# Performance work log

Measured on AMD Instinct MI355X. Metric: run time of the kernel, lower is better.

Reference implementation:

```python
import math
import jax, jax.numpy as jnp
import numpy as np

B_IN, B_OUT = 16, 16
F_IN, F_OUT, BATCH = 32, 64, 4
N_ALPHA, N_GAMMA = 4, 3
KERNEL_BETA = math.pi / 8.0
L_TOT = sum((2 * l + 1) ** 2 for l in range(B_OUT))  # 5456


def _lg(n):
    return math.lgamma(n + 1.0)


def _small_d(l, beta):
    """Wigner small-d matrix d^l_{m,n}(beta), [2l+1, 2l+1], Condon-Shortley phase."""
    c, s = math.cos(0.5 * beta), math.sin(0.5 * beta)
    d = np.zeros((2 * l + 1, 2 * l + 1), dtype=np.float64)
    for mi, m in enumerate(range(-l, l + 1)):
        for ni, n in enumerate(range(-l, l + 1)):
            pref = 0.5 * (_lg(l + m) + _lg(l - m) + _lg(l + n) + _lg(l - n))
            acc = 0.0
            for k in range(max(0, n - m), min(l + n, l - m) + 1):
                ln = pref - _lg(l + n - k) - _lg(k) - _lg(m - n + k) - _lg(l - m - k)
                acc += ((-1.0) ** (m - n + k)) * math.exp(ln) * (c ** (2 * l + n - m - 2 * k)) * (s ** (m - n + 2 * k))
            d[mi, ni] = acc
    return d


def _qweights(b):
    """Kostelec-Rockmore SOFT quadrature weights over the 2b beta samples."""
    k = np.arange(b)
    w = np.array([
        (2.0 / b) * math.sin(math.pi * (2 * j + 1) / (4.0 * b)) *
        np.sum(np.sin((2 * j + 1) * (2 * k + 1) * math.pi / (4.0 * b)) / (2 * k + 1))
        for j in range(2 * b)])
    return w


def _wigner_table(betas, b_out, scale_fn):
    rows = []
    for beta in betas:
        blocks = [(_small_d(l, beta) * scale_fn(l)).ravel() for l in range(b_out)]
        rows.append(np.concatenate(blocks))
    return np.stack(rows)  # [len(betas), L_TOT]


def _grid_basis(grid, b_out):
    """conj(D^l_{mn}(a,b,g)) = e^{+i m a} d^l_{mn}(b) e^{+i n g}, flattened over (l,m,n)."""
    cols = []
    for (a, bb, g) in grid:
        blocks = []
        for l in range(b_out):
            m = np.arange(-l, l + 1)
            d = _small_d(l, bb)
            ph = np.exp(1j * (m[:, None] * a + m[None, :] * g))
            blocks.append((d * ph).ravel())
        cols.append(np.concatenate(blocks))
    return np.stack(cols, axis=1)  # [L_TOT, n_grid] complex


def _freq_indices(b_out, nfft):
    ms, ns = [], []
    for l in range(b_out):
        r = np.arange(-l, l + 1)
        M, N = np.meshgrid(r, r, indexing='ij')
        ms.append(np.mod(M.ravel(), nfft))
        ns.append(np.mod(N.ravel(), nfft))
    return np.concatenate(ms), np.concatenate(ns)


def make_grid():
    alphas = [2.0 * math.pi * i / N_ALPHA for i in range(N_ALPHA)]
    gammas = [2.0 * math.pi * i / N_GAMMA for i in range(N_GAMMA)]
    return [(a, KERNEL_BETA, g) for a in alphas for g in gammas]


def setup_inputs() -> dict:
    key = jax.random.key(0)
    k1, k2 = jax.random.split(key)
    x = jax.random.normal(k1, (BATCH, F_IN, 2 * B_IN, 2 * B_IN, 2 * B_IN), jnp.float32)
    grid = make_grid()
    n_grid = len(grid)
    stdv = 1.0 / math.sqrt(n_grid * F_IN * (B_OUT ** 3) / float(B_IN ** 3))
    kernel = stdv * jax.random.normal(k2, (F_IN, F_OUT, n_grid), jnp.float32)
    bias = jnp.zeros((1, F_OUT, 1, 1, 1), jnp.float32)
    # analysis table: quadrature weight * d, with (2pi/2b)^2/(8pi^2) = 1/(8 b^2) absorbed
    betas_in = np.pi * (2 * np.arange(2 * B_IN) + 1) / (4.0 * B_IN)
    w = _qweights(B_IN) / (8.0 * B_IN ** 2)
    wig_f = _wigner_table(betas_in, B_OUT, lambda l: 1.0) * w[:, None]
    # synthesis table: (2l+1) * d, times (2b)^2 to cancel ifft2 normalization
    betas_out = np.pi * (2 * np.arange(2 * B_OUT) + 1) / (4.0 * B_OUT)
    wig_i = _wigner_table(betas_out, B_OUT, lambda l: (2 * l + 1) * (2 * B_OUT) ** 2)
    D = _grid_basis(grid, B_OUT)
    return {
        'x': x, 'kernel': kernel, 'bias': bias,
        'wigner_fwd': jnp.asarray(wig_f, jnp.float32),
        'wigner_inv': jnp.asarray(wig_i, jnp.float32),
        'D_re': jnp.asarray(D.real, jnp.float32),
        'D_im': jnp.asarray(D.imag, jnp.float32),
    }


def reference(x, kernel, bias, wigner_fwd, wigner_inv, D_re, D_im):
    batch, fin = x.shape[0], x.shape[1]
    fout = kernel.shape[1]
    midx_in, nidx_in = _freq_indices(B_OUT, 2 * B_IN)
    midx_out, nidx_out = _freq_indices(B_OUT, 2 * B_OUT)
    # --- SO3 FFT of input: FFT over (alpha, gamma), weighted beta-sum with Wigner-d ---
    Xf = jnp.fft.fft2(x.astype(jnp.complex64), axes=(-2, -1))   # [z,i,beta,ma,ng]
    Xg = Xf[..., midx_in, nidx_in]                               # [z,i,beta,L]
    xh = jnp.einsum('bl,zibl->lzi', wigner_fwd.astype(jnp.complex64), Xg)  # [L,z,i]
    # --- local FT of kernel on SO(3) grid points ---
    Dc = jax.lax.complex(D_re, D_im)                             # [L, n_grid]
    yh = jnp.einsum('lj,ioj->lio', Dc, kernel.astype(jnp.complex64))       # [L,i,o]
    # --- per-frequency block matmul (SO3_mm): z^l = x^l @ y^l, contracting f_in ---
    zs, begin = [], 0
    for l in range(B_OUT):
        n = 2 * l + 1
        xl = xh[begin:begin + n * n].reshape(n, n, batch, fin)
        yl = yh[begin:begin + n * n].reshape(n, n, fin, fout)
        zs.append(jnp.einsum('mkzi,knio->mnzo', xl, yl).reshape(n * n, batch, fout))
        begin += n * n
    zh = jnp.concatenate(zs, axis=0)                             # [L,z,o]
    # --- inverse SO3 FFT: scatter (l,m,n) -> FFT bins, ifft over (alpha,gamma) ---
    term = jnp.einsum('bl,lzo->zobl', wigner_inv.astype(jnp.complex64), zh)
    ng = 2 * B_OUT
    Zf = jnp.zeros((batch, fout, ng, ng, ng), jnp.complex64)
    Zf = Zf.at[..., midx_out, nidx_out].add(term)
    out = jnp.fft.ifft2(Zf, axes=(-2, -1)).real.astype(x.dtype)
    return out + bias
```

## Files before the change

kernel.cpp:

```cpp
#include <hip/hip_runtime.h>
#include <math.h>


typedef unsigned short u16;
typedef unsigned int   u32;
typedef __attribute__((ext_vector_type(8))) short  short8;
typedef __attribute__((ext_vector_type(4))) float  floatx4;
typedef __attribute__((ext_vector_type(2))) float  f32x2;

constexpr int LTOT = 5456;

constexpr int LB[17] = {0,1,10,35,84,165,286,455,680,969,
                        1330,1771,2300,2925,3654,4495,5456};

__device__ inline u16 f2bf(float f) {
    u32 u = __float_as_uint(f);
    u += 0x7fff + ((u >> 16) & 1);
    return (u16)(u >> 16);
}
__device__ inline u32 pack2bf(float re, float im) {
    return (u32)f2bf(re) | ((u32)f2bf(im) << 16);
}

__device__ inline short8 btr4(uint4 q, u32 sel, u32 msk) {
    uint4 t;
    t.x = __builtin_amdgcn_perm(q.x, q.x, sel) ^ msk;
    t.y = __builtin_amdgcn_perm(q.y, q.y, sel) ^ msk;
    t.z = __builtin_amdgcn_perm(q.z, q.z, sel) ^ msk;
    t.w = __builtin_amdgcn_perm(q.w, q.w, sel) ^ msk;
    return *(short8*)&t;
}

__device__ __forceinline__ f32x2 cfma(f32x2 e, f32x2 t, f32x2 acc) {
    asm("v_pk_fma_f32 %0, %1, %2, %0 op_sel:[0,0,0] op_sel_hi:[0,1,1]\n\t"
        "v_pk_fma_f32 %0, %1, %2, %0 op_sel:[1,1,0] op_sel_hi:[1,0,1] neg_lo:[0,1,0]"
        : "+v"(acc) : "v"(e), "v"(t));
    return acc;
}
__device__ __forceinline__ f32x2 cmulp(f32x2 t, f32x2 r) {
    f32x2 d;
    asm("v_pk_mul_f32 %0, %1, %2 op_sel:[0,0] op_sel_hi:[0,1]\n\t"
        "v_pk_fma_f32 %0, %1, %2, %0 op_sel:[1,1,0] op_sel_hi:[1,0,1] neg_lo:[0,1,0]"
        : "=&v"(d) : "v"(t), "v"(r));
    return d;
}
__device__ __forceinline__ f32x2 fma_bl(f32x2 w2, f32x2 v, f32x2 acc) {
    asm("v_pk_fma_f32 %0, %1, %2, %0 op_sel:[0,0,0] op_sel_hi:[0,1,1]"
        : "+v"(acc) : "v"(w2), "v"(v));
    return acc;
}
__device__ __forceinline__ f32x2 fma_bh(f32x2 w2, f32x2 v, f32x2 acc) {
    asm("v_pk_fma_f32 %0, %1, %2, %0 op_sel:[1,0,0] op_sel_hi:[1,1,1]"
        : "+v"(acc) : "v"(w2), "v"(v));
    return acc;
}

__global__ __launch_bounds__(256) void k_wtr(const float* __restrict__ w,
                                             float* __restrict__ wT) {
    int t  = blockIdx.x * 256 + threadIdx.x;
    int bq = blockIdx.y;
    if (t < LTOT) {
        float4 v;
        v.x = w[(size_t)(bq * 4 + 0) * LTOT + t];
        v.y = w[(size_t)(bq * 4 + 1) * LTOT + t];
        v.z = w[(size_t)(bq * 4 + 2) * LTOT + t];
        v.w = w[(size_t)(bq * 4 + 3) * LTOT + t];
        *(float4*)(wT + ((size_t)bq * LTOT + t) * 4) = v;
    }
}

__global__ __launch_bounds__(512) void k_fft_fwd(const float* __restrict__ x,
                                                 u32* __restrict__ Xfb) {
    __shared__ __align__(8) float xs[1088];
    __shared__ __align__(8) f32x2 Gc[1056];
    __shared__ f32x2 Wfc[32];
    int tid = threadIdx.x;
    if (tid < 32) {
        float sv, cv;
        sincosf(6.28318530717958647692f * (float)tid / 32.0f, &sv, &cv);
        f32x2 wv; wv.x = cv; wv.y = -sv;
        Wfc[tid] = wv;
    }
    const float* src = x + (size_t)blockIdx.x * 1024;
    for (int e = tid; e < 1024; e += 512) xs[(e >> 5) * 34 + (e & 31)] = src[e];
    __syncthreads();
    {
        int a = tid >> 4, k = tid & 15;
        const f32x2* rowp = (const f32x2*)&xs[a * 34];
        f32x2 r = Wfc[2 * k];
        f32x2 p0 = rowp[0];
        f32x2 E; E.x = p0.x; E.y = 0.f;
        f32x2 O; O.x = p0.y; O.y = 0.f;
        f32x2 t = r;
#pragma unroll
        for (int h = 1; h < 16; h++) {
            f32x2 p = rowp[h];
            E = fma_bl(p, t, E);
            O = fma_bh(p, t, O);
            if (h < 15) t = cmulp(t, r);
        }
        f32x2 WO = cmulp(O, Wfc[k]);
        Gc[a * 33 + k]      = E + WO;
        Gc[a * 33 + k + 16] = E - WO;
    }
    __syncthreads();
    {
        u32* dst = Xfb + (size_t)blockIdx.x * 512;
        int ng = tid & 31, ma = tid >> 5;
        f32x2 r = Wfc[2 * ma];
        f32x2 E = Gc[ng];
        f32x2 O = Gc[33 + ng];
        f32x2 t = r;
#pragma unroll
        for (int h = 1; h < 16; h++) {
            f32x2 e = Gc[(2 * h) * 33 + ng];
            f32x2 o = Gc[(2 * h + 1) * 33 + ng];
            E = cfma(e, t, E);
            O = cfma(o, t, O);
            if (h < 15) t = cmulp(t, r);
        }
        f32x2 WO = cmulp(O, Wfc[ma]);
        dst[ma * 32 + ng] = pack2bf(E.x + WO.x, E.y + WO.y);
    }
}

__global__ __launch_bounds__(256) void k_prep_B(const float* __restrict__ Dre,
                                                const float* __restrict__ Dim,
                                                const float* __restrict__ ker,
                                                u32* __restrict__ yhb) {
    __shared__ float Ds[2][24];
    int t0  = blockIdx.x * 2;
    int tid = threadIdx.x;
    if (tid < 48) {
        int rr = tid / 24, jj = tid - rr * 24;
        Ds[rr][jj] = (jj < 12) ? Dre[(t0 + rr) * 12 + jj] : Dim[(t0 + rr) * 12 + jj - 12];
    }
    __syncthreads();
    for (int rep = 0; rep < 8; rep++) {
        int io = rep * 256 + tid;
        int i  = io >> 6, o = io & 63;
        int nio = ((i >> 4) << 10) + ((o >> 5) << 9) + (((o >> 3) & 3) << 7)
                + (((i >> 2) & 3) << 5) + ((o & 7) << 2) + (i & 3);
        const float4* kp = (const float4*)(ker + io * 12);
        float4 ka = kp[0], kb = kp[1], kc = kp[2];
        float kv[12] = {ka.x, ka.y, ka.z, ka.w, kb.x, kb.y, kb.z, kb.w,
                        kc.x, kc.y, kc.z, kc.w};
#pragma unroll
        for (int rr = 0; rr < 2; rr++) {
            float sr = 0.f, si = 0.f;
#pragma unroll
            for (int j = 0; j < 12; j++) {
                sr += Ds[rr][j]      * kv[j];
                si += Ds[rr][12 + j] * kv[j];
            }
            yhb[(size_t)(t0 + rr) * 2048 + nio] = pack2bf(sr, si);
        }
    }
}

__global__ __launch_bounds__(256) void k_beta_A(const u32* __restrict__ Xfb,
                                                const float* __restrict__ wfT,
                                                u16* __restrict__ Ab) {
    int ma  = blockIdx.x >> 6;
    int zig = blockIdx.x & 63;
    int tid = threadIdx.x;
    int ng  = tid & 31;
    int lq  = (tid >> 5) & 3;
    int zil = tid >> 7;
    int zi  = zig * 2 + zil;
    int z = zi >> 5, i = zi & 31;
    int mh = (ma <= 15) ? ma : ma - 32;
    int nh = (ng <= 15) ? ng : ng - 32;
    int am = mh < 0 ? -mh : mh;
    int an = nh < 0 ? -nh : nh;
    int l0 = am > an ? am : an;
    int lb = lq * 4;

    int isconj = (ma > 16);
    int mau = isconj ? (32 - ma) : ma;
    int ngu = isconj ? ((32 - ng) & 31) : ng;
    if (mau > 15) { mau = 0; ngu = 0; }

    int tl[4];
#pragma unroll
    for (int j = 0; j < 4; j++) {
        int l = lb + j;
        tl[j] = LB[l] + (mh + l) * (2 * l + 1) + (nh + l);
    }
    float2 acc[4];
#pragma unroll
    for (int j = 0; j < 4; j++) acc[j] = make_float2(0.f, 0.f);

    const u32* xp = Xfb + (size_t)zi * 32 * 512 + mau * 32 + ngu;
    float sgn = isconj ? -1.f : 1.f;
#pragma unroll 2
    for (int bq = 0; bq < 8; bq++) {
        u32 p0 = xp[(size_t)(4 * bq + 0) * 512];
        u32 p1 = xp[(size_t)(4 * bq + 1) * 512];
        u32 p2 = xp[(size_t)(4 * bq + 2) * 512];
        u32 p3 = xp[(size_t)(4 * bq + 3) * 512];
        float vx0 = __uint_as_float(p0 << 16);
        float vy0 = sgn * __uint_as_float(p0 & 0xffff0000u);
        float vx1 = __uint_as_float(p1 << 16);
        float vy1 = sgn * __uint_as_float(p1 & 0xffff0000u);
        float vx2 = __uint_as_float(p2 << 16);
        float vy2 = sgn * __uint_as_float(p2 & 0xffff0000u);
        float vx3 = __uint_as_float(p3 << 16);
        float vy3 = sgn * __uint_as_float(p3 & 0xffff0000u);
        const float4* wq = (const float4*)(wfT + (size_t)bq * (LTOT * 4));
#pragma unroll
        for (int j = 0; j < 4; j++) {
            if (lb + j >= l0) {
                float4 w = wq[tl[j]];
                acc[j].x += w.x * vx0 + w.y * vx1 + w.z * vx2 + w.w * vx3;
                acc[j].y += w.x * vy0 + w.y * vy1 + w.z * vy2 + w.w * vy3;
            }
        }
    }
    int s_i  = i >> 4;
    int kl   = 2 * (i & 15);
    int joff = kl & 7;
    int Lhi  = (kl >> 3) << 4;
#pragma unroll
    for (int j = 0; j < 4; j++) {
        int l = lb + j;
        if (l >= l0) {
            int mi = mh + l, ni = nh + l;
            int s   = 2 * ni + s_i;
            int row = 4 * mi + z;
            u32 pack = pack2bf(acc[j].x, acc[j].y);
            size_t off = (size_t)8192 * l * l + (size_t)s * 4096
                       + ((row >> 4) << 9) + ((Lhi + (row & 15)) << 3) + joff;
            *(u32*)(Ab + off) = pack;
        }
    }
}

__global__ __launch_bounds__(256) void k_gemm(const u16* __restrict__ Ab,
                                              const u32* __restrict__ yhb,
                                              float* __restrict__ zhT) {
    int id  = (int)blockIdx.x;
    int o5  = id & 31;
    int g   = o5 & 7;
    int k5  = o5 >> 3;
    int flat = (id & ~31) | ((g & 3) + ((g >> 2) << 4) + (k5 << 2));
    int rem = flat, l, nl = 1;
    for (l = 15; l >= 0; l--) {
        nl = 2 * l + 1;
        int c = nl * 4;
        if (rem < c) break;
        rem -= c;
    }
    int n  = rem >> 2;
    int oq = rem & 3;
    int base = LB[l];
    const u16* Ag = Ab + (size_t)8192 * l * l;
    int S = 2 * nl;

    int tid = threadIdx.x, lane = tid & 63, w = tid >> 6;
    int cc = lane & 1;
    u32 sel = cc ? 0x01000302u : 0x03020100u;
    u32 msk = cc ? 0u          : 0x80000000u;

    const u32* Bb = yhb + (size_t)(base + n) * 2048 + (oq << 8) + ((lane >> 1) << 2);
    const u16* Aw = Ag + ((w << 10) | (lane << 3));

    floatx4 acc[2][2];
#pragma unroll
    for (int a = 0; a < 2; a++)
#pragma unroll
        for (int b = 0; b < 2; b++) acc[a][b] = (floatx4)0.f;

#define LOADB(s, q0, q1) { \
    const uint4* bp = (const uint4*)(Bb + (size_t)((s) >> 1) * nl * 2048 + (((s) & 1) << 10)); \
    q0 = bp[0]; q1 = bp[32]; }
#define LOADA(s, r0, r1) { \
    const u16* apx = Aw + (size_t)(s) * 4096; \
    r0 = *(const short8*)apx; r1 = *(const short8*)(apx + 512); }
#define MF(a, b, c) __builtin_amdgcn_mfma_f32_16x16x32_bf16(a, b, c, 0, 0, 0)
#define COMP2REFILL(Bx0, Bx1, Ax0, Ax1, By0, By1, Ay0, Ay1, snew) { \
    short8 bf0 = btr4(Bx0, sel, msk), bf1 = btr4(Bx1, sel, msk); \
    short8 af0 = Ax0, af1 = Ax1; \
    short8 cf0 = btr4(By0, sel, msk), cf1 = btr4(By1, sel, msk); \
    short8 ag0 = Ay0, ag1 = Ay1; \
    LOADA(snew, Ax0, Ax1); LOADB(snew, Bx0, Bx1); \
    LOADA((snew) + 1, Ay0, Ay1); LOADB((snew) + 1, By0, By1); \
    acc[0][0] = MF(af0, bf0, acc[0][0]);  acc[1][0] = MF(af1, bf0, acc[1][0]); \
    acc[0][1] = MF(af0, bf1, acc[0][1]);  acc[1][1] = MF(af1, bf1, acc[1][1]); \
    acc[0][0] = MF(ag0, cf0, acc[0][0]);  acc[1][0] = MF(ag1, cf0, acc[1][0]); \
    acc[0][1] = MF(ag0, cf1, acc[0][1]);  acc[1][1] = MF(ag1, cf1, acc[1][1]); }

    uint4 p0B0, p0B1, p0C0, p0C1; short8 p0a0, p0a1, p0c0, p0c1;
    uint4 p1B0, p1B1, p1C0, p1C1; short8 p1a0, p1a1, p1c0, p1c1;
    LOADA(0, p0a0, p0a1); LOADB(0, p0B0, p0B1);
    LOADA(1, p0c0, p0c1); LOADB(1, p0C0, p0C1);
    LOADA(2, p1a0, p1a1); LOADB(2, p1B0, p1B1);
    LOADA(3, p1c0, p1c1); LOADB(3, p1C0, p1C1);

    COMP2REFILL(p0B0, p0B1, p0a0, p0a1, p0C0, p0C1, p0c0, p0c1, 4);
    for (int s = 2; s + 2 < S; s += 4) {
        COMP2REFILL(p1B0, p1B1, p1a0, p1a1, p1C0, p1C1, p1c0, p1c1, s + 4);
        COMP2REFILL(p0B0, p0B1, p0a0, p0a1, p0C0, p0C1, p0c0, p0c1, s + 6);
    }
#undef COMP2REFILL
#undef LOADB
#undef LOADA
#undef MF

    int q = lane >> 4, cn = lane & 15;
#pragma unroll
    for (int mt = 0; mt < 2; mt++) {
#pragma unroll
        for (int nt = 0; nt < 2; nt++) {
            int nu2 = (nt << 4) + cn;
            int o2  = (oq << 4) + (nu2 >> 1);
            int c2  = nu2 & 1;
#pragma unroll
            for (int r = 0; r < 4; r++) {
                int R = (w << 5) + (mt << 4) + (q << 2) + r;
                int m = R >> 2, z = R & 3;
                if (m < nl) {
                    int t  = base + m * nl + n;
                    int zo = (z << 6) + o2;
                    zhT[((size_t)zo * LTOT + t) * 2 + c2] = acc[mt][nt][r];
                }
            }
        }
    }
}

__global__ __launch_bounds__(256, 8) void k_inv2(const float2* __restrict__ zhT,
                                                 const float* __restrict__ wiT,
                                                 const float* __restrict__ bias,
                                                 float* __restrict__ out) {
    __shared__ __align__(16) f32x2 Pb[4 * 544];
    __shared__ f32x2 Wf[32];
    int tid = threadIdx.x;
    int zo = blockIdx.x & 255;
    int bq = blockIdx.x >> 8;
    int b0 = bq * 4;
    if (tid < 32) {
        float sv, cv;
        sincosf(6.28318530717958647692f * (float)tid / 32.0f, &sv, &cv);
        f32x2 wv; wv.x = cv; wv.y = sv;
        Wf[tid] = wv;
    }
    {
        int ng = tid & 31, rq = tid >> 5;
        int nh = (ng <= 15) ? ng : ng - 32;
        int an = nh < 0 ? -nh : nh;
        const f32x2* zr = (const f32x2*)zhT + (size_t)zo * LTOT;
        const f32x2* wp = (const f32x2*)wiT + (size_t)bq * (LTOT * 2);
#pragma unroll
        for (int mr = 0; mr < 2; mr++) {
            int ma = rq + 8 * mr;
            int l0 = ma > an ? ma : an;
            f32x2 a0 = (f32x2)0.f, a1 = a0, a2 = a0, a3 = a0;
#pragma unroll 4
            for (int l = 0; l < 16; l++) {
                if (l >= l0) {
                    int t = LB[l] + (ma + l) * (2 * l + 1) + (nh + l);
                    f32x2 zv = zr[t];
                    f32x2 w01 = wp[2 * t], w23 = wp[2 * t + 1];
                    a0 = fma_bl(w01, zv, a0);
                    a1 = fma_bh(w01, zv, a1);
                    a2 = fma_bl(w23, zv, a2);
                    a3 = fma_bh(w23, zv, a3);
                }
            }
            int po = ma * 34 + ng;
            Pb[po]            = a0;
            Pb[544 + po]      = a1;
            Pb[2 * 544 + po]  = a2;
            Pb[3 * 544 + po]  = a3;
        }
    }
    __syncthreads();
#pragma unroll
    for (int it = 0; it < 2; it++) {
        int task = tid + it * 256;
        int rowid = task >> 3, q = task & 7;
        f32x2* prow = &Pb[(rowid >> 4) * 544 + (rowid & 15) * 34];
        const floatx4* prow4 = (const floatx4*)prow;
        floatx4 eo0 = prow4[0];
        f32x2 Ep; Ep.x = eo0.x; Ep.y = eo0.y;
        f32x2 Op; Op.x = eo0.z; Op.y = eo0.w;
        f32x2 En = (f32x2)0.f, On = (f32x2)0.f;
        f32x2 r = Wf[2 * q];
        f32x2 t = r;
#pragma unroll
        for (int h = 1; h < 16; h++) {
            floatx4 eo = prow4[h];
            f32x2 e; e.x = eo.x; e.y = eo.y;
            f32x2 o; o.x = eo.z; o.y = eo.w;
            if (h & 1) { En = cfma(e, t, En); On = cfma(o, t, On); }
            else       { Ep = cfma(e, t, Ep); Op = cfma(o, t, Op); }
            if (h < 15) t = cmulp(t, r);
        }
        f32x2 E0 = Ep + En, E1 = Ep - En;
        f32x2 O0 = Op + On, O1 = Op - On;
        f32x2 wq = Wf[q];
        f32x2 w0 = cmulp(O0, wq);
        f32x2 u1 = cmulp(O1, wq);
        f32x2 w1; w1.x = -u1.y; w1.y = u1.x;
        prow[q]      = E0 + w0;
        prow[q + 16] = E0 - w0;
        prow[q + 8]  = E1 + w1;
        prow[q + 24] = E1 - w1;
    }
    __syncthreads();
    float bv = bias[zo & 63];
#pragma unroll
    for (int it = 0; it < 4; it++) {
        int task = tid + it * 256;
        int p = task >> 8, rr = task & 255;
        int qa = rr >> 5, g = rr & 31;
        const f32x2* pc = &Pb[p * 544];
        f32x2 r = Wf[2 * qa];
        f32x2 u = Wf[qa];
        f32x2 Uee = (f32x2)0.f, Ueo = Uee, Ve = Uee, Vo = Uee;
        f32x2 c0 = pc[g];
        {
            f32x2 c1 = pc[34 + g];
            Ve = cfma(c1, u, Ve);
        }
        f32x2 t = r;
        u = cmulp(u, r);
#pragma unroll
        for (int j = 1; j < 8; j++) {
            f32x2 ce = pc[(2 * j) * 34 + g];
            f32x2 co = pc[(2 * j + 1) * 34 + g];
            if (j & 1) { Ueo = cfma(ce, t, Ueo); Vo = cfma(co, u, Vo); }
            else       { Uee = cfma(ce, t, Uee); Ve = cfma(co, u, Ve); }
            if (j < 7) { t = cmulp(t, r); u = cmulp(u, r); }
        }
        float EaA = c0.x + 2.f * (Uee.x + Ueo.x);
        float EaB = c0.x + 2.f * (Uee.x - Ueo.x);
        float OaA = 2.f * (Ve.x + Vo.x);
        float OaB = -2.f * (Ve.y - Vo.y);
        float* dst = out + (size_t)zo * 32768 + (size_t)(b0 + p) * 1024;
        constexpr float sc = 1.f / 1024.f;
        dst[qa * 32 + g]         = (EaA + OaA) * sc + bv;
        dst[(qa + 16) * 32 + g]  = (EaA - OaA) * sc + bv;
        dst[(qa + 8) * 32 + g]   = (EaB + OaB) * sc + bv;
        dst[(qa + 24) * 32 + g]  = (EaB - OaB) * sc + bv;
    }
}

extern "C" void kernel_launch(void* const* d_in, const int* in_sizes, int n_in,
                              void* d_out, int out_size, void* d_ws, size_t ws_size,
                              hipStream_t stream) {
    const float* x    = (const float*)d_in[0];
    const float* ker  = (const float*)d_in[1];
    const float* bias = (const float*)d_in[2];
    const float* wf   = (const float*)d_in[3];
    const float* wi   = (const float*)d_in[4];
    const float* Dre  = (const float*)d_in[5];
    const float* Dim  = (const float*)d_in[6];
    float* out = (float*)d_out;

    char* ws = (char*)d_ws;
    u32*    yhb = (u32*)ws;
    u16*    Ab  = (u16*)(ws + 44695552);
    float*  zhT = (float*)(ws + 44695552 + 4194304);
    u32*    Xfb = (u32*)zhT;
    float*  wfT = (float*)(ws + 44695552 + 4194304 + 8388608);
    float*  wiT = (float*)ws;

    hipLaunchKernelGGL(k_fft_fwd, dim3(4096),  dim3(512), 0, stream, x, Xfb);
    hipLaunchKernelGGL(k_wtr,     dim3(22, 8), dim3(256), 0, stream, wf, wfT);
    hipLaunchKernelGGL(k_prep_B,  dim3(2728),  dim3(256), 0, stream, Dre, Dim, ker, yhb);
    hipLaunchKernelGGL(k_beta_A,  dim3(2048),  dim3(256), 0, stream, Xfb, wfT, Ab);
    hipLaunchKernelGGL(k_gemm,    dim3(1024),  dim3(256), 0, stream, Ab, yhb, zhT);
    hipLaunchKernelGGL(k_wtr,     dim3(22, 8), dim3(256), 0, stream, wi, wiT);
    hipLaunchKernelGGL(k_inv2,    dim3(2048),  dim3(256), 0, stream,
                       (const float2*)zhT, wiT, bias, out);
}
```

Baseline: 200.7 us.

## Stage B operand tiles through double-buffered shared memory in SO3 block GEMM

```diff
diff --git a/kernel.cpp b/kernel.cpp
--- a/kernel.cpp
+++ b/kernel.cpp
@@ -239,11 +239,13 @@
 __global__ __launch_bounds__(256) void k_gemm(const u16* __restrict__ Ab,
                                               const u32* __restrict__ yhb,
                                               float* __restrict__ zhT) {
+    __shared__ __align__(16) uint4 Bs[2][128];
+
     int id  = (int)blockIdx.x;
     int o5  = id & 31;
-    int g   = o5 & 7;
+    int g5  = o5 & 7;
     int k5  = o5 >> 3;
-    int flat = (id & ~31) | ((g & 3) + ((g >> 2) << 4) + (k5 << 2));
+    int flat = (id & ~31) | ((g5 & 3) + ((g5 >> 2) << 4) + (k5 << 2));
     int rem = flat, l, nl = 1;
     for (l = 15; l >= 0; l--) {
         nl = 2 * l + 1;
@@ -255,15 +257,16 @@
     int oq = rem & 3;
     int base = LB[l];
     const u16* Ag = Ab + (size_t)8192 * l * l;
-    int S = 2 * nl;
+    int G = nl;
 
     int tid = threadIdx.x, lane = tid & 63, w = tid >> 6;
     int cc = lane & 1;
     u32 sel = cc ? 0x01000302u : 0x03020100u;
     u32 msk = cc ? 0u          : 0x80000000u;
 
-    const u32* Bb = yhb + (size_t)(base + n) * 2048 + (oq << 8) + ((lane >> 1) << 2);
-    const u16* Aw = Ag + ((w << 10) | (lane << 3));
+    const uint4* Bg = (const uint4*)yhb + (size_t)(base + n) * 512 + (oq << 6);
+    const u16*   Aw = Ag + ((w << 10) | (lane << 3));
+    int lu = tid & 63, lsl = tid >> 6;
 
     floatx4 acc[2][2];
 #pragma unroll
@@ -271,40 +274,44 @@
 #pragma unroll
         for (int b = 0; b < 2; b++) acc[a][b] = (floatx4)0.f;
 
-#define LOADB(s, q0, q1) { \
-    const uint4* bp = (const uint4*)(Bb + (size_t)((s) >> 1) * nl * 2048 + (((s) & 1) << 10)); \
-    q0 = bp[0]; q1 = bp[32]; }
-#define LOADA(s, r0, r1) { \
-    const u16* apx = Aw + (size_t)(s) * 4096; \
-    r0 = *(const short8*)apx; r1 = *(const short8*)(apx + 512); }
+#define LOADBG(gg, br) { if (tid < 128) br = Bg[(size_t)(gg) * nl * 512 + (lsl << 8) + lu]; }
+#define LOADA2(gg, r0, r1, r2, r3) { \
+    const u16* apx = Aw + (size_t)(gg) * 8192; \
+    r0 = *(const short8*)apx;          r1 = *(const short8*)(apx + 512); \
+    r2 = *(const short8*)(apx + 4096); r3 = *(const short8*)(apx + 4608); }
 #define MF(a, b, c) __builtin_amdgcn_mfma_f32_16x16x32_bf16(a, b, c, 0, 0, 0)
-#define COMP2REFILL(Bx0, Bx1, Ax0, Ax1, By0, By1, Ay0, Ay1, snew) { \
-    short8 bf0 = btr4(Bx0, sel, msk), bf1 = btr4(Bx1, sel, msk); \
-    short8 af0 = Ax0, af1 = Ax1; \
-    short8 cf0 = btr4(By0, sel, msk), cf1 = btr4(By1, sel, msk); \
-    short8 ag0 = Ay0, ag1 = Ay1; \
-    LOADA(snew, Ax0, Ax1); LOADB(snew, Bx0, Bx1); \
-    LOADA((snew) + 1, Ay0, Ay1); LOADB((snew) + 1, By0, By1); \
-    acc[0][0] = MF(af0, bf0, acc[0][0]);  acc[1][0] = MF(af1, bf0, acc[1][0]); \
-    acc[0][1] = MF(af0, bf1, acc[0][1]);  acc[1][1] = MF(af1, bf1, acc[1][1]); \
-    acc[0][0] = MF(ag0, cf0, acc[0][0]);  acc[1][0] = MF(ag1, cf0, acc[1][0]); \
-    acc[0][1] = MF(ag0, cf1, acc[0][1]);  acc[1][1] = MF(ag1, cf1, acc[1][1]); }
-
-    uint4 p0B0, p0B1, p0C0, p0C1; short8 p0a0, p0a1, p0c0, p0c1;
-    uint4 p1B0, p1B1, p1C0, p1C1; short8 p1a0, p1a1, p1c0, p1c1;
-    LOADA(0, p0a0, p0a1); LOADB(0, p0B0, p0B1);
-    LOADA(1, p0c0, p0c1); LOADB(1, p0C0, p0C1);
-    LOADA(2, p1a0, p1a1); LOADB(2, p1B0, p1B1);
-    LOADA(3, p1c0, p1c1); LOADB(3, p1C0, p1C1);
-
-    COMP2REFILL(p0B0, p0B1, p0a0, p0a1, p0C0, p0C1, p0c0, p0c1, 4);
-    for (int s = 2; s + 2 < S; s += 4) {
-        COMP2REFILL(p1B0, p1B1, p1a0, p1a1, p1C0, p1C1, p1c0, p1c1, s + 4);
-        COMP2REFILL(p0B0, p0B1, p0a0, p0a1, p0C0, p0C1, p0c0, p0c1, s + 6);
-    }
-#undef COMP2REFILL
-#undef LOADB
-#undef LOADA
+#define GROUP(buf, A0r, A1r, A2r, A3r, gnext) { \
+    __syncthreads(); \
+    if (tid < 128) Bs[(buf) ^ 1][tid] = Br; \
+    LOADBG(gnext, Br); \
+    short8 la0 = A0r, la1 = A1r, la2 = A2r, la3 = A3r; \
+    LOADA2(gnext, A0r, A1r, A2r, A3r); \
+    uint4 q0 = Bs[buf][lane >> 1],       q1 = Bs[buf][32 + (lane >> 1)]; \
+    uint4 q2 = Bs[buf][64 + (lane >> 1)], q3 = Bs[buf][96 + (lane >> 1)]; \
+    short8 bf0 = btr4(q0, sel, msk), bf1 = btr4(q1, sel, msk); \
+    short8 bf2 = btr4(q2, sel, msk), bf3 = btr4(q3, sel, msk); \
+    acc[0][0] = MF(la0, bf0, acc[0][0]);  acc[1][0] = MF(la1, bf0, acc[1][0]); \
+    acc[0][1] = MF(la0, bf1, acc[0][1]);  acc[1][1] = MF(la1, bf1, acc[1][1]); \
+    acc[0][0] = MF(la2, bf2, acc[0][0]);  acc[1][0] = MF(la3, bf2, acc[1][0]); \
+    acc[0][1] = MF(la2, bf3, acc[0][1]);  acc[1][1] = MF(la3, bf3, acc[1][1]); }
+
+    uint4 Br;
+    short8 e0, e1, e2, e3;
+    short8 d0, d1, d2, d3;
+    LOADBG(0, Br);
+    if (tid < 128) Bs[0][tid] = Br;
+    LOADBG(1, Br);
+    LOADA2(0, e0, e1, e2, e3);
+    LOADA2(1, d0, d1, d2, d3);
+
+    GROUP(0, e0, e1, e2, e3, 2);
+    for (int g = 1; g + 1 < G; g += 2) {
+        GROUP(1, d0, d1, d2, d3, g + 2);
+        GROUP(0, e0, e1, e2, e3, g + 3);
+    }
+#undef GROUP
+#undef LOADBG
+#undef LOADA2
 #undef MF
 
     int q = lane >> 4, cn = lane & 15;
```

Result: faster. 193.0 us (-3.8%).
